# Performance work log

Hardware: AMD Instinct MI355X
Metric: run time of the kernel (lower is better)

## Reference

```python
import jax, jax.numpy as jnp
import numpy as np

EPS = 1e-5
GROUPS = 32

# 3x3 regular grid: row0 = dy, row1 = dx for kernel index k = ky*3 + kx
_REG = jnp.array([[-1, -1, -1, 0, 0, 0, 1, 1, 1],
                  [-1, 0, 1, -1, 0, 1, -1, 0, 1]], dtype=jnp.float32)


def conv2d(x, w, pad):
    return jax.lax.conv_general_dilated(
        x, w, window_strides=(1, 1), padding=((pad, pad), (pad, pad)),
        dimension_numbers=('NCHW', 'OIHW', 'NCHW'))


def deform_conv3x3(x, off_y, off_x, w_dcn, dilation):
    # x: (N,C,H,W); off_y/off_x: (N,H,W,9); w_dcn: (Cout,Cin,3,3)
    N, C, H, W = x.shape
    dyk = (jnp.arange(9) // 3 - 1).astype(jnp.float32) * dilation  # (9,)
    dxk = (jnp.arange(9) % 3 - 1).astype(jnp.float32) * dilation
    yy = jnp.arange(H, dtype=jnp.float32)
    xx = jnp.arange(W, dtype=jnp.float32)
    # sampling positions (padding == dilation, stride == 1)
    py = yy[None, :, None, None] + dyk[None, None, None, :] + off_y  # (N,H,W,9)
    px = xx[None, None, :, None] + dxk[None, None, None, :] + off_x

    y0 = jnp.floor(py)
    x0 = jnp.floor(px)
    wy1 = py - y0
    wx1 = px - x0

    xflat = x.reshape(N, C, H * W)

    def gather(xf, idx):  # xf (C,HW), idx (H,W,9) -> (C,H,W,9)
        return xf[:, idx]

    val = jnp.zeros((N, C, H, W, 9), dtype=x.dtype)
    corners = [
        (y0, x0, (1.0 - wy1) * (1.0 - wx1)),
        (y0, x0 + 1.0, (1.0 - wy1) * wx1),
        (y0 + 1.0, x0, wy1 * (1.0 - wx1)),
        (y0 + 1.0, x0 + 1.0, wy1 * wx1),
    ]
    for yc, xc, wc in corners:
        valid = ((yc >= 0) & (yc <= H - 1) & (xc >= 0) & (xc <= W - 1)).astype(x.dtype)
        yi = jnp.clip(yc, 0, H - 1).astype(jnp.int32)
        xi = jnp.clip(xc, 0, W - 1).astype(jnp.int32)
        ind = yi * W + xi  # (N,H,W,9)
        g = jax.vmap(gather)(xflat, ind)  # (N,C,H,W,9)
        val = val + g * (wc * valid)[:, None]

    Cout = w_dcn.shape[0]
    wk = w_dcn.reshape(Cout, C, 9)
    return jnp.einsum('nchwk,ock->nohw', val, wk)


def group_norm(x, gamma, beta, groups, eps):
    N, C, H, W = x.shape
    xg = x.reshape(N, groups, C // groups, H, W)
    mu = xg.mean(axis=(2, 3, 4), keepdims=True)
    var = xg.var(axis=(2, 3, 4), keepdims=True)
    xn = ((xg - mu) * jax.lax.rsqrt(var + eps)).reshape(N, C, H, W)
    return xn * gamma[None, :, None, None] + beta[None, :, None, None]


def setup_inputs() -> dict:
    key = jax.random.key(0)
    k1, k2, k3, k4 = jax.random.split(key, 4)
    C, Cout = 256, 256
    x = jax.random.normal(k1, (8, C, 64, 64), dtype=jnp.float32)
    w_tm = jax.random.normal(k2, (4, C, 3, 3), dtype=jnp.float32) * 0.02
    b_tm = jnp.zeros((4,), dtype=jnp.float32)
    w_dcn = jax.random.normal(k3, (Cout, C, 3, 3), dtype=jnp.float32) * 0.02
    gn_gamma = jnp.ones((Cout,), dtype=jnp.float32)
    gn_beta = jnp.zeros((Cout,), dtype=jnp.float32)
    return {"x": x, "w_tm": w_tm, "b_tm": b_tm, "w_dcn": w_dcn,
            "gn_gamma": gn_gamma, "gn_beta": gn_beta}


def reference(x, w_tm, b_tm, w_dcn, gn_gamma, gn_beta):
    N, C, H, W = x.shape
    # offset-generating 3x3 conv -> 4 channels = per-pixel 2x2 transform matrix
    tm = conv2d(x, w_tm, pad=1) + b_tm[None, :, None, None]  # (N,4,H,W)
    T = tm.transpose(0, 2, 3, 1).reshape(N, H, W, 2, 2)
    off = jnp.einsum('nhwij,jk->nhwik', T, _REG) - _REG  # (N,H,W,2,9)
    off_y = off[..., 0, :]  # (N,H,W,9)
    off_x = off[..., 1, :]
    out = deform_conv3x3(x, off_y, off_x, w_dcn, dilation=1)
    out = group_norm(out, gn_gamma, gn_beta, GROUPS, EPS)
    return jax.nn.relu(out)
```

## Files before the change

### kernel.cpp

```cpp
#include <hip/hip_runtime.h>
#include <hip/hip_fp16.h>
#include <stdint.h>

typedef float        f32x4 __attribute__((ext_vector_type(4)));
typedef _Float16     f16x8 __attribute__((ext_vector_type(8)));
typedef _Float16     f16x2 __attribute__((ext_vector_type(2)));
typedef _Float16 f16;

__device__ inline float bf2f(unsigned short b){ return __builtin_bit_cast(float,(unsigned)b<<16); }
__device__ inline bool is_bf16_mode(const void* g){ return ((const unsigned*)g)[0]==0x3F803F80u; }
__device__ inline float ld_in(const void* p, int i, bool bfm){
  return bfm ? bf2f(((const unsigned short*)p)[i]) : ((const float*)p)[i];
}

#if defined(__has_builtin)
#if __has_builtin(__builtin_amdgcn_fdot2)
#define HAS_FDOT2 1
#endif
#endif
#ifdef HAS_FDOT2
#define FDOT2(acc,a,b) (acc = __builtin_amdgcn_fdot2((a),(b),(acc),false))
#else
#define FDOT2(acc,a,b) (acc += (float)(a)[0]*(float)(b)[0] + (float)(a)[1]*(float)(b)[1])
#endif

#define FAST_BARRIER() __asm__ __volatile__("s_waitcnt lgkmcnt(0)\n\ts_barrier" ::: "memory")

#define WS_XT   0u
#define WS_BF   16777216u
#define WS_ST   17956864u
#define WS_NEED 17958912u

__device__ inline int wslot(int tap, int cp){ return (tap*128 + cp) ^ ((cp >> 2) & 7); }

__global__ __launch_bounds__(256) void k_prep(const void* __restrict__ x_,
                                              const void* __restrict__ wdcn,
                                              const void* __restrict__ gamma,
                                              f16* __restrict__ xt,
                                              f16* __restrict__ Bf,
                                              float* __restrict__ stats){
  const bool bfm = is_bf16_mode(gamma);
  const int t = threadIdx.x;
  if (blockIdx.y == 4){
    if (blockIdx.x == 0 && blockIdx.z == 0){
      stats[t] = 0.f; stats[t + 256] = 0.f;
    }
    int base = (blockIdx.z*64 + blockIdx.x)*256 + t;
    #pragma unroll
    for (int it = 0; it < 5; it++){
      int i = base + it*131072;
      if (i < 589824){
        int u    = i & 7;
        int l    = (i >> 3)  & 63;
        int tile = (i >> 9)  & 15;
        int ks   = (i >> 13) & 1;
        int ch   = (i >> 14) & 3;
        int tap  = i >> 16;
        int ml = l & 15, q = l >> 4;
        int oc = tile*16 + ml;
        int c  = ch*64 + ks*32 + q*8 + u;
        Bf[i] = (f16)ld_in(wdcn, oc*2304 + c*9 + tap, bfm);
      }
    }
    return;
  }
  __shared__ float tile[64][65];
  const int n  = blockIdx.z;
  const int c0 = blockIdx.y << 6;
  const int s0 = blockIdx.x << 6;
  {
    const int sp = (t & 31) * 2;
    const int q  = t >> 5;
    #pragma unroll
    for (int i = 0; i < 8; i++){
      int cc = q + i*8;
      int base = (n*256 + c0 + cc)*4096 + s0 + sp;
      tile[cc][sp]   = ld_in(x_, base,   bfm);
      tile[cc][sp+1] = ld_in(x_, base+1, bfm);
    }
  }
  __syncthreads();
  {
    const int cc = (t & 31) * 2;
    const int q  = t >> 5;
    f16* dst = xt + (size_t)(n*4096 + s0)*256 + c0;
    #pragma unroll
    for (int i = 0; i < 8; i++){
      int s = q + i*8;
      dst[s*256 + cc]   = (f16)tile[cc][s];
      dst[s*256 + cc+1] = (f16)tile[cc+1][s];
    }
  }
}

#define KSTEP(STEP, BC, BN, PAR) do {                                                   \
  if ((STEP) < 35){                       \
    const int tap1 = ((STEP)+1) >> 2, ch1 = ((STEP)+1) & 3;                             \
    _Pragma("unroll") for (int ks = 0; ks < 2; ks++)                                    \
      _Pragma("unroll") for (int nt = 0; nt < 4; nt++)                                  \
        BN[ks][nt] = *(const f16x8*)(Bf + (((((tap1*4+ch1)*2+ks)*16) + (wid*4+nt)) << 9) + l*8); \
  }                                                                                     \
  {                                             \
    f16* dst = &At[(PAR)*4608 + bpx*72];                                                \
    const f16 wA=(f16)cwf.x, wB=(f16)cwf.y, wC=(f16)cwf.z, wD=(f16)cwf.w;               \
    _Pragma("unroll") for (int cc = 0; cc < 2; cc++){                                   \
      f16x8 R = pA[cc]*wA + pB[cc]*wB + pC[cc]*wC + pD[cc]*wD;                          \
      *(f16x8*)(dst + (cc*4 + bcq)*8) = R;                                              \
    }                                                                                   \
  }                                                                                     \
  if ((STEP) < 35){                                  \
    const int s1 = (STEP) + 1;                                                          \
    const int e = (s1 >> 2)*64 + bpx;                                                   \
    const int4 id = idxL[e];                                                            \
    cwf = wfL[e];                                                                       \
    _Pragma("unroll") for (int cc = 0; cc < 2; cc++){                                   \
      const int cb = ((s1 & 3)*64 + (cc*4 + bcq)*8)*2;                                  \
      pA[cc] = *(const f16x8*)(xb + id.x + cb);                                         \
      pB[cc] = *(const f16x8*)(xb + id.y + cb);                                         \
      pC[cc] = *(const f16x8*)(xb + id.z + cb);                                         \
      pD[cc] = *(const f16x8*)(xb + id.w + cb);                                         \
    }                                                                                   \
  }                                                                                     \
  FAST_BARRIER();                                                                       \
  { const f16* Atr = &At[(PAR)*4608];                                                   \
    _Pragma("unroll") for (int ks = 0; ks < 2; ks++){                                   \
      f16x8 afr[4];                                                                     \
      _Pragma("unroll") for (int mt = 0; mt < 4; mt++)                                  \
        afr[mt] = *(const f16x8*)(Atr + (mt*16 + ml)*72 + ks*32 + q*8);                 \
      _Pragma("unroll") for (int mt = 0; mt < 4; mt++)                                  \
        _Pragma("unroll") for (int nt = 0; nt < 4; nt++)                                \
          acc[mt][nt] = __builtin_amdgcn_mfma_f32_16x16x32_f16(afr[mt], BC[ks][nt], acc[mt][nt], 0, 0, 0); \
    } }                                                                                 \
} while(0)

__global__ __launch_bounds__(256,2) void k_fused8(const f16* __restrict__ xt,
                                                  const f16* __restrict__ Bf,
                                                  const void* __restrict__ wtm_,
                                                  const void* __restrict__ btm_,
                                                  const void* __restrict__ gamma,
                                                  float* __restrict__ out,
                                                  float* __restrict__ stats){
  __shared__ __attribute__((aligned(16))) char smemA[18432];
  __shared__ float4 wfL[576];
  __shared__ int4   idxL[576];
  __shared__ float4 Tsm[64];
  f16* wh = (f16*)smemA;
  f16* At = (f16*)smemA;
  const bool bfm = is_bf16_mode(gamma);
  const int t = threadIdx.x;
  const int blk = blockIdx.x;
  const int n = blk & 7, h = blk >> 3;
  const int wid = t >> 6, l = t & 63;
  const int ml = l & 15, q = l >> 4;

  for (int i = t; i < 9216; i += 256){
    int o = i / 2304, r = i % 2304, c = r / 9, tap = r % 9;
    int cp = c >> 1;
    wh[wslot(tap, cp)*8 + o*2 + (c & 1)] = (f16)ld_in(wtm_, i, bfm);
  }
  __syncthreads();

  {
    const int px = t >> 2, cq = t & 3;
    float a0=0.f, a1=0.f, a2=0.f, a3=0.f;
    for (int tap = 0; tap < 9; tap++){
      const int yy = h + tap/3 - 1, xx = px + tap%3 - 1;
      if ((unsigned)yy < 64u && (unsigned)xx < 64u){
        const f16* row = xt + ((n*4096 + yy*64 + xx)*256);
        #pragma unroll
        for (int jb = 0; jb < 8; jb++){
          const int chunk = jb*4 + cq;
          f16x8 xv = *(const f16x8*)(row + chunk*8);
          #pragma unroll
          for (int p = 0; p < 4; p++){
            const int cp = chunk*4 + p;
            const f16x8 W = *(const f16x8*)&wh[wslot(tap, cp)*8];
            const f16x2 xp = {xv[2*p], xv[2*p+1]};
            FDOT2(a0, xp, ((f16x2){W[0], W[1]}));
            FDOT2(a1, xp, ((f16x2){W[2], W[3]}));
            FDOT2(a2, xp, ((f16x2){W[4], W[5]}));
            FDOT2(a3, xp, ((f16x2){W[6], W[7]}));
          }
        }
      }
    }
    a0 += __shfl_xor(a0,1,64); a0 += __shfl_xor(a0,2,64);
    a1 += __shfl_xor(a1,1,64); a1 += __shfl_xor(a1,2,64);
    a2 += __shfl_xor(a2,1,64); a2 += __shfl_xor(a2,2,64);
    a3 += __shfl_xor(a3,1,64); a3 += __shfl_xor(a3,2,64);
    if (cq == 0){
      float4 r;
      r.x = a0 + ld_in(btm_,0,bfm);  r.y = a1 + ld_in(btm_,1,bfm);
      r.z = a2 + ld_in(btm_,2,bfm);  r.w = a3 + ld_in(btm_,3,bfm);
      Tsm[px] = r;
    }
  }
  __syncthreads();

  for (int e = t; e < 576; e += 256){
    const int px = e & 63, tap = e >> 6;
    const float4 T = Tsm[px];
    const float dy = (float)(tap/3 - 1);
    const float dx = (float)(tap%3 - 1);
    float py  = (float)h  + T.x*dy + T.y*dx;
    float pxx = (float)px + T.z*dy + T.w*dx;
    float y0 = floorf(py), x0 = floorf(pxx);
    float wy = py - y0,  wx = pxx - x0;
    float y1 = y0 + 1.f, x1 = x0 + 1.f;
    float vy0 = (y0 >= 0.f && y0 <= 63.f) ? 1.f : 0.f;
    float vy1 = (y1 >= 0.f && y1 <= 63.f) ? 1.f : 0.f;
    float vx0 = (x0 >= 0.f && x0 <= 63.f) ? 1.f : 0.f;
    float vx1 = (x1 >= 0.f && x1 <= 63.f) ? 1.f : 0.f;
    float4 wf;
    wf.x = (1.f-wy)*(1.f-wx)*vy0*vx0;
    wf.y = (1.f-wy)*wx      *vy0*vx1;
    wf.z = wy*(1.f-wx)      *vy1*vx0;
    wf.w = wy*wx            *vy1*vx1;
    int yi0 = (int)fminf(fmaxf(y0,0.f),63.f);
    int yi1 = (int)fminf(fmaxf(y1,0.f),63.f);
    int xi0 = (int)fminf(fmaxf(x0,0.f),63.f);
    int xi1 = (int)fminf(fmaxf(x1,0.f),63.f);
    const int base = n*4096*512;
    int4 id;
    id.x = base + (yi0*64 + xi0)*512;
    id.y = base + (yi0*64 + xi1)*512;
    id.z = base + (yi1*64 + xi0)*512;
    id.w = base + (yi1*64 + xi1)*512;
    idxL[e] = id;
    wfL[e]  = wf;
  }

  f32x4 acc[4][4];
  #pragma unroll
  for (int mt = 0; mt < 4; mt++)
    #pragma unroll
    for (int nt = 0; nt < 4; nt++) acc[mt][nt] = (f32x4){0.f,0.f,0.f,0.f};

  const int bpx = t >> 2, bcq = t & 3;
  const char* xb = (const char*)xt;

  __syncthreads();

  f16x8 bA[2][4], bB[2][4];
  #pragma unroll
  for (int ks = 0; ks < 2; ks++)
    #pragma unroll
    for (int nt = 0; nt < 4; nt++)
      bA[ks][nt] = *(const f16x8*)(Bf + (((ks*16) + (wid*4 + nt)) << 9) + l*8);

  f16x8 pA[2], pB[2], pC[2], pD[2]; float4 cwf;
  {
    const int4 id = idxL[bpx];
    cwf = wfL[bpx];
    #pragma unroll
    for (int cc = 0; cc < 2; cc++){
      const int cb = ((cc*4 + bcq)*8)*2;
      pA[cc] = *(const f16x8*)(xb + id.x + cb);
      pB[cc] = *(const f16x8*)(xb + id.y + cb);
      pC[cc] = *(const f16x8*)(xb + id.z + cb);
      pD[cc] = *(const f16x8*)(xb + id.w + cb);
    }
  }

  for (int s2 = 0; s2 < 36; s2 += 2){
    KSTEP(s2,     bA, bB, 0);
    KSTEP(s2 + 1, bB, bA, 1);
  }

  #pragma unroll
  for (int mt = 0; mt < 4; mt++)
    #pragma unroll
    for (int nt = 0; nt < 4; nt++){
      const int oc = wid*64 + nt*16 + ml;
      const int m0 = mt*16 + q*4;
      float4 v;
      v.x = acc[mt][nt][0]; v.y = acc[mt][nt][1];
      v.z = acc[mt][nt][2]; v.w = acc[mt][nt][3];
      *(float4*)(out + (size_t)(n*256 + oc)*4096 + h*64 + m0) = v;
    }
  #pragma unroll
  for (int nt = 0; nt < 4; nt++){
    float s1 = 0.f, s2 = 0.f;
    #pragma unroll
    for (int mt = 0; mt < 4; mt++)
      #pragma unroll
      for (int rr = 0; rr < 4; rr++){
        float v = acc[mt][nt][rr];
        s1 += v; s2 += v*v;
      }
    s1 += __shfl_xor(s1,16,64); s1 += __shfl_xor(s1,32,64);
    s2 += __shfl_xor(s2,16,64); s2 += __shfl_xor(s2,32,64);
    s1 += __shfl_xor(s1,1,64);  s1 += __shfl_xor(s1,2,64);  s1 += __shfl_xor(s1,4,64);
    s2 += __shfl_xor(s2,1,64);  s2 += __shfl_xor(s2,2,64);  s2 += __shfl_xor(s2,4,64);
    if ((l & 0x37) == 0){
      const int oc = wid*64 + nt*16 + (l & 8);
      const int g = oc >> 3;
      atomicAdd(stats + n*64 + g*2,     s1);
      atomicAdd(stats + n*64 + g*2 + 1, s2);
    }
  }
}

__global__ __launch_bounds__(256) void k_gn(float* __restrict__ out,
                                            const float* __restrict__ stats,
                                            const void* __restrict__ gamma,
                                            const void* __restrict__ beta){
  const int blk = blockIdx.x;
  const int n = blk >> 8, oc = blk & 255;
  const int g = oc >> 3;
  const bool bfm = is_bf16_mode(gamma);
  const float s1 = stats[n*64 + g*2];
  const float s2 = stats[n*64 + g*2 + 1];
  const float inv = 1.f/32768.f;
  const float mu  = s1*inv;
  const float var = s2*inv - mu*mu;
  const float rs  = rsqrtf(var + 1e-5f);
  const float gv = ld_in(gamma, oc, bfm);
  const float bv = ld_in(beta,  oc, bfm);
  const float sc = gv*rs;
  const float sh = bv - mu*sc;
  float* p = out + (size_t)(n*256 + oc)*4096;
  const int t = threadIdx.x;
  #pragma unroll
  for (int i = 0; i < 4; i++){
    float4 v = *(float4*)(p + (i*256 + t)*4);
    v.x = fmaxf(v.x*sc + sh, 0.f);
    v.y = fmaxf(v.y*sc + sh, 0.f);
    v.z = fmaxf(v.z*sc + sh, 0.f);
    v.w = fmaxf(v.w*sc + sh, 0.f);
    *(float4*)(p + (i*256 + t)*4) = v;
  }
}

__global__ void k_ws_small(float* out){ if (threadIdx.x == 0) out[0] += 200000.f; }

extern "C" void kernel_launch(void* const* d_in, const int* in_sizes, int n_in,
                              void* d_out, int out_size, void* d_ws, size_t ws_size,
                              hipStream_t stream){
  const void* x     = d_in[0];
  const void* wtm   = d_in[1];
  const void* btm   = d_in[2];
  const void* wdcn  = d_in[3];
  const void* gamma = d_in[4];
  const void* beta  = d_in[5];
  float* out = (float*)d_out;
  if (ws_size < (size_t)WS_NEED){
    hipLaunchKernelGGL(k_ws_small, dim3(1), dim3(64), 0, stream, out);
    return;
  }
  char* ws = (char*)d_ws;
  f16*   xt    = (f16*)  (ws + WS_XT);
  f16*   Bf    = (f16*)  (ws + WS_BF);
  float* stats = (float*)(ws + WS_ST);

  hipLaunchKernelGGL(k_prep,   dim3(64,5,8), dim3(256), 0, stream, x, wdcn, gamma, xt, Bf, stats);
  hipLaunchKernelGGL(k_fused8, dim3(512),    dim3(256), 0, stream, xt, Bf, wtm, btm, gamma, out, stats);
  hipLaunchKernelGGL(k_gn,     dim3(2048),   dim3(256), 0, stream, out, stats, gamma, beta);
}
```

Measured before the change: 187.8 us.

## Split K across wave pairs with 512-thread blocks in fused deform-conv kernel

Doubles the block to 512 threads. The two halves of the waves each take one k-slice of every 64-channel step, and their partial accumulators are summed through shared memory before the output stores and GroupNorm statistics. The offset conv and the bilinear gather are spread over 8 threads per pixel instead of 4. The previous register double-buffering of B fragments and gathered pixels is replaced by a simpler loop that loads them in the same step they are used. The aim is more waves in flight to hide gather latency, at the cost of extra reduction syncs and less software prefetch.

```diff
diff --git a/kernel.cpp b/kernel.cpp
--- a/kernel.cpp
+++ b/kernel.cpp
@@ -93,47 +93,7 @@
   }
 }
 
-#define KSTEP(STEP, BC, BN, PAR) do {                                                   \
-  if ((STEP) < 35){                       \
-    const int tap1 = ((STEP)+1) >> 2, ch1 = ((STEP)+1) & 3;                             \
-    _Pragma("unroll") for (int ks = 0; ks < 2; ks++)                                    \
-      _Pragma("unroll") for (int nt = 0; nt < 4; nt++)                                  \
-        BN[ks][nt] = *(const f16x8*)(Bf + (((((tap1*4+ch1)*2+ks)*16) + (wid*4+nt)) << 9) + l*8); \
-  }                                                                                     \
-  {                                             \
-    f16* dst = &At[(PAR)*4608 + bpx*72];                                                \
-    const f16 wA=(f16)cwf.x, wB=(f16)cwf.y, wC=(f16)cwf.z, wD=(f16)cwf.w;               \
-    _Pragma("unroll") for (int cc = 0; cc < 2; cc++){                                   \
-      f16x8 R = pA[cc]*wA + pB[cc]*wB + pC[cc]*wC + pD[cc]*wD;                          \
-      *(f16x8*)(dst + (cc*4 + bcq)*8) = R;                                              \
-    }                                                                                   \
-  }                                                                                     \
-  if ((STEP) < 35){                                  \
-    const int s1 = (STEP) + 1;                                                          \
-    const int e = (s1 >> 2)*64 + bpx;                                                   \
-    const int4 id = idxL[e];                                                            \
-    cwf = wfL[e];                                                                       \
-    _Pragma("unroll") for (int cc = 0; cc < 2; cc++){                                   \
-      const int cb = ((s1 & 3)*64 + (cc*4 + bcq)*8)*2;                                  \
-      pA[cc] = *(const f16x8*)(xb + id.x + cb);                                         \
-      pB[cc] = *(const f16x8*)(xb + id.y + cb);                                         \
-      pC[cc] = *(const f16x8*)(xb + id.z + cb);                                         \
-      pD[cc] = *(const f16x8*)(xb + id.w + cb);                                         \
-    }                                                                                   \
-  }                                                                                     \
-  FAST_BARRIER();                                                                       \
-  { const f16* Atr = &At[(PAR)*4608];                                                   \
-    _Pragma("unroll") for (int ks = 0; ks < 2; ks++){                                   \
-      f16x8 afr[4];                                                                     \
-      _Pragma("unroll") for (int mt = 0; mt < 4; mt++)                                  \
-        afr[mt] = *(const f16x8*)(Atr + (mt*16 + ml)*72 + ks*32 + q*8);                 \
-      _Pragma("unroll") for (int mt = 0; mt < 4; mt++)                                  \
-        _Pragma("unroll") for (int nt = 0; nt < 4; nt++)                                \
-          acc[mt][nt] = __builtin_amdgcn_mfma_f32_16x16x32_f16(afr[mt], BC[ks][nt], acc[mt][nt], 0, 0, 0); \
-    } }                                                                                 \
-} while(0)
-
-__global__ __launch_bounds__(256,2) void k_fused8(const f16* __restrict__ xt,
+__global__ __launch_bounds__(512,4) void k_fused8(const f16* __restrict__ xt,
                                                   const f16* __restrict__ Bf,
                                                   const void* __restrict__ wtm_,
                                                   const void* __restrict__ btm_,
@@ -151,25 +111,32 @@
   const int blk = blockIdx.x;
   const int n = blk & 7, h = blk >> 3;
   const int wid = t >> 6, l = t & 63;
+  const int wc = wid & 3, ks = wid >> 2;
   const int ml = l & 15, q = l >> 4;
 
-  for (int i = t; i < 9216; i += 256){
-    int o = i / 2304, r = i % 2304, c = r / 9, tap = r % 9;
-    int cp = c >> 1;
-    wh[wslot(tap, cp)*8 + o*2 + (c & 1)] = (f16)ld_in(wtm_, i, bfm);
+  for (int s = t; s < 1152; s += 512){
+    const int tap = s >> 7, cp = s & 127;
+    const int c = cp*2;
+    f16x8 W;
+    #pragma unroll
+    for (int o = 0; o < 4; o++){
+      W[o*2]   = (f16)ld_in(wtm_, o*2304 + c*9 + tap,     bfm);
+      W[o*2+1] = (f16)ld_in(wtm_, o*2304 + (c+1)*9 + tap, bfm);
+    }
+    *(f16x8*)(wh + wslot(tap, cp)*8) = W;
   }
   __syncthreads();
 
   {
-    const int px = t >> 2, cq = t & 3;
+    const int px = t >> 3, cq = t & 7;
     float a0=0.f, a1=0.f, a2=0.f, a3=0.f;
     for (int tap = 0; tap < 9; tap++){
       const int yy = h + tap/3 - 1, xx = px + tap%3 - 1;
       if ((unsigned)yy < 64u && (unsigned)xx < 64u){
         const f16* row = xt + ((n*4096 + yy*64 + xx)*256);
         #pragma unroll
-        for (int jb = 0; jb < 8; jb++){
-          const int chunk = jb*4 + cq;
+        for (int jb = 0; jb < 4; jb++){
+          const int chunk = jb*8 + cq;
           f16x8 xv = *(const f16x8*)(row + chunk*8);
           #pragma unroll
           for (int p = 0; p < 4; p++){
@@ -184,10 +151,10 @@
         }
       }
     }
-    a0 += __shfl_xor(a0,1,64); a0 += __shfl_xor(a0,2,64);
-    a1 += __shfl_xor(a1,1,64); a1 += __shfl_xor(a1,2,64);
-    a2 += __shfl_xor(a2,1,64); a2 += __shfl_xor(a2,2,64);
-    a3 += __shfl_xor(a3,1,64); a3 += __shfl_xor(a3,2,64);
+    a0 += __shfl_xor(a0,1,64); a0 += __shfl_xor(a0,2,64); a0 += __shfl_xor(a0,4,64);
+    a1 += __shfl_xor(a1,1,64); a1 += __shfl_xor(a1,2,64); a1 += __shfl_xor(a1,4,64);
+    a2 += __shfl_xor(a2,1,64); a2 += __shfl_xor(a2,2,64); a2 += __shfl_xor(a2,4,64);
+    a3 += __shfl_xor(a3,1,64); a3 += __shfl_xor(a3,2,64); a3 += __shfl_xor(a3,4,64);
     if (cq == 0){
       float4 r;
       r.x = a0 + ld_in(btm_,0,bfm);  r.y = a1 + ld_in(btm_,1,bfm);
@@ -197,7 +164,7 @@
   }
   __syncthreads();
 
-  for (int e = t; e < 576; e += 256){
+  for (int e = t; e < 576; e += 512){
     const int px = e & 63, tap = e >> 6;
     const float4 T = Tsm[px];
     const float dy = (float)(tap/3 - 1);
@@ -236,67 +203,102 @@
     #pragma unroll
     for (int nt = 0; nt < 4; nt++) acc[mt][nt] = (f32x4){0.f,0.f,0.f,0.f};
 
-  const int bpx = t >> 2, bcq = t & 3;
+  const int bpx = t >> 3, bu = t & 7;
   const char* xb = (const char*)xt;
 
   __syncthreads();
 
-  f16x8 bA[2][4], bB[2][4];
-  #pragma unroll
-  for (int ks = 0; ks < 2; ks++)
+  int4  idc = idxL[bpx];
+  float4 cwf = wfL[bpx];
+
+  for (int step = 0; step < 36; step++){
+    const int tap = step >> 2, ch = step & 3;
+    f16x8 bfr[4];
     #pragma unroll
     for (int nt = 0; nt < 4; nt++)
-      bA[ks][nt] = *(const f16x8*)(Bf + (((ks*16) + (wid*4 + nt)) << 9) + l*8);
-
-  f16x8 pA[2], pB[2], pC[2], pD[2]; float4 cwf;
-  {
-    const int4 id = idxL[bpx];
-    cwf = wfL[bpx];
-    #pragma unroll
-    for (int cc = 0; cc < 2; cc++){
-      const int cb = ((cc*4 + bcq)*8)*2;
-      pA[cc] = *(const f16x8*)(xb + id.x + cb);
-      pB[cc] = *(const f16x8*)(xb + id.y + cb);
-      pC[cc] = *(const f16x8*)(xb + id.z + cb);
-      pD[cc] = *(const f16x8*)(xb + id.w + cb);
-    }
-  }
-
-  for (int s2 = 0; s2 < 36; s2 += 2){
-    KSTEP(s2,     bA, bB, 0);
-    KSTEP(s2 + 1, bB, bA, 1);
-  }
-
-  #pragma unroll
-  for (int mt = 0; mt < 4; mt++)
-    #pragma unroll
-    for (int nt = 0; nt < 4; nt++){
-      const int oc = wid*64 + nt*16 + ml;
-      const int m0 = mt*16 + q*4;
-      float4 v;
-      v.x = acc[mt][nt][0]; v.y = acc[mt][nt][1];
-      v.z = acc[mt][nt][2]; v.w = acc[mt][nt][3];
-      *(float4*)(out + (size_t)(n*256 + oc)*4096 + h*64 + m0) = v;
-    }
+      bfr[nt] = *(const f16x8*)(Bf + ((((tap*4+ch)*2 + ks)*16 + (wc*4+nt)) << 9) + l*8);
+    const int cb = (ch*64 + bu*8)*2;
+    f16x8 gA = *(const f16x8*)(xb + idc.x + cb);
+    f16x8 gB = *(const f16x8*)(xb + idc.y + cb);
+    f16x8 gC = *(const f16x8*)(xb + idc.z + cb);
+    f16x8 gD = *(const f16x8*)(xb + idc.w + cb);
+    {
+      const f16 wA=(f16)cwf.x, wB=(f16)cwf.y, wC=(f16)cwf.z, wD=(f16)cwf.w;
+      f16x8 R = gA*wA + gB*wB + gC*wC + gD*wD;
+      *(f16x8*)(&At[(step & 1)*4608 + bpx*72 + bu*8]) = R;
+    }
+    if ((step & 3) == 3 && step < 35){
+      const int e = ((step+1) >> 2)*64 + bpx;
+      idc = idxL[e];
+      cwf = wfL[e];
+    }
+    FAST_BARRIER();
+    const f16* Atr = &At[(step & 1)*4608];
+    #pragma unroll
+    for (int mt = 0; mt < 4; mt++){
+      f16x8 afr = *(const f16x8*)(Atr + (mt*16 + ml)*72 + ks*32 + q*8);
+      #pragma unroll
+      for (int nt = 0; nt < 4; nt++)
+        acc[mt][nt] = __builtin_amdgcn_mfma_f32_16x16x32_f16(afr, bfr[nt], acc[mt][nt], 0, 0, 0);
+    }
+  }
+
+  float4* red = (float4*)smemA;
   #pragma unroll
   for (int nt = 0; nt < 4; nt++){
-    float s1 = 0.f, s2 = 0.f;
+    __syncthreads();
+    if (ks == 1){
+      #pragma unroll
+      for (int k = 0; k < 4; k++){
+        float4 v;
+        v.x = acc[k][nt][0]; v.y = acc[k][nt][1];
+        v.z = acc[k][nt][2]; v.w = acc[k][nt][3];
+        red[wc*256 + k*64 + l] = v;
+      }
+    }
+    __syncthreads();
+    if (ks == 0){
+      #pragma unroll
+      for (int k = 0; k < 4; k++){
+        float4 v = red[wc*256 + k*64 + l];
+        acc[k][nt][0] += v.x; acc[k][nt][1] += v.y;
+        acc[k][nt][2] += v.z; acc[k][nt][3] += v.w;
+      }
+    }
+  }
+
+  if (ks == 0){
     #pragma unroll
     for (int mt = 0; mt < 4; mt++)
       #pragma unroll
-      for (int rr = 0; rr < 4; rr++){
-        float v = acc[mt][nt][rr];
-        s1 += v; s2 += v*v;
-      }
-    s1 += __shfl_xor(s1,16,64); s1 += __shfl_xor(s1,32,64);
-    s2 += __shfl_xor(s2,16,64); s2 += __shfl_xor(s2,32,64);
-    s1 += __shfl_xor(s1,1,64);  s1 += __shfl_xor(s1,2,64);  s1 += __shfl_xor(s1,4,64);
-    s2 += __shfl_xor(s2,1,64);  s2 += __shfl_xor(s2,2,64);  s2 += __shfl_xor(s2,4,64);
-    if ((l & 0x37) == 0){
-      const int oc = wid*64 + nt*16 + (l & 8);
-      const int g = oc >> 3;
-      atomicAdd(stats + n*64 + g*2,     s1);
-      atomicAdd(stats + n*64 + g*2 + 1, s2);
+      for (int nt = 0; nt < 4; nt++){
+        const int oc = wc*64 + nt*16 + ml;
+        const int m0 = mt*16 + q*4;
+        float4 v;
+        v.x = acc[mt][nt][0]; v.y = acc[mt][nt][1];
+        v.z = acc[mt][nt][2]; v.w = acc[mt][nt][3];
+        *(float4*)(out + (size_t)(n*256 + oc)*4096 + h*64 + m0) = v;
+      }
+    #pragma unroll
+    for (int nt = 0; nt < 4; nt++){
+      float s1 = 0.f, s2 = 0.f;
+      #pragma unroll
+      for (int mt = 0; mt < 4; mt++)
+        #pragma unroll
+        for (int rr = 0; rr < 4; rr++){
+          float v = acc[mt][nt][rr];
+          s1 += v; s2 += v*v;
+        }
+      s1 += __shfl_xor(s1,16,64); s1 += __shfl_xor(s1,32,64);
+      s2 += __shfl_xor(s2,16,64); s2 += __shfl_xor(s2,32,64);
+      s1 += __shfl_xor(s1,1,64);  s1 += __shfl_xor(s1,2,64);  s1 += __shfl_xor(s1,4,64);
+      s2 += __shfl_xor(s2,1,64);  s2 += __shfl_xor(s2,2,64);  s2 += __shfl_xor(s2,4,64);
+      if ((l & 0x37) == 0){
+        const int oc = wc*64 + nt*16 + (l & 8);
+        const int g = oc >> 3;
+        atomicAdd(stats + n*64 + g*2,     s1);
+        atomicAdd(stats + n*64 + g*2 + 1, s2);
+      }
     }
   }
 }
@@ -354,6 +356,6 @@
   float* stats = (float*)(ws + WS_ST);
 
   hipLaunchKernelGGL(k_prep,   dim3(64,5,8), dim3(256), 0, stream, x, wdcn, gamma, xt, Bf, stats);
-  hipLaunchKernelGGL(k_fused8, dim3(512),    dim3(256), 0, stream, xt, Bf, wtm, btm, gamma, out, stats);
+  hipLaunchKernelGGL(k_fused8, dim3(512),    dim3(512), 0, stream, xt, Bf, wtm, btm, gamma, out, stats);
   hipLaunchKernelGGL(k_gn,     dim3(2048),   dim3(256), 0, stream, out, stats, gamma, beta);
 }
```

Measured after the change: 182.6 us. -2.8%, faster.
